# Kernel optimization log

Measured on AMD Instinct MI355X. Metric: run time of the kernel, lower is better.

Reference implementation:

```python
import jax, jax.numpy as jnp
import numpy as np

N = 16384          # num nodes
E = 262144         # num edges (before self loops)
IN_DIM = 128
HID = 128
OUT = 2
TRIM = 0.1
MAX_DEG = 48       # padded max in-degree (incl. self loop); safe bound for Poisson(16)+1
BN_EPS = 1e-5


def _lin_params(key, fan_in, fan_out):
    kw, kb = jax.random.split(key)
    s = 1.0 / np.sqrt(fan_in)
    W = jax.random.uniform(kw, (fan_in, fan_out), jnp.float32, -s, s)
    b = jax.random.uniform(kb, (fan_out,), jnp.float32, -s, s)
    return W, b


def setup_inputs() -> dict:
    key = jax.random.key(0)
    ks = jax.random.split(key, 8)
    x = jax.random.normal(ks[0], (N, IN_DIM), jnp.float32)
    edge_index = jax.random.randint(ks[1], (2, E), 0, N, jnp.int32)
    Wl0, bl0 = _lin_params(ks[2], IN_DIM, HID)
    Wr0, br0 = _lin_params(ks[3], IN_DIM, HID)
    Wl1, bl1 = _lin_params(ks[4], HID, HID)
    Wr1, br1 = _lin_params(ks[5], HID, HID)
    Wl2, bl2 = _lin_params(ks[6], HID, OUT)
    Wr2, br2 = _lin_params(ks[7], HID, OUT)
    g0 = jnp.ones((HID,), jnp.float32); be0 = jnp.zeros((HID,), jnp.float32)
    g1 = jnp.ones((HID,), jnp.float32); be1 = jnp.zeros((HID,), jnp.float32)
    return dict(x=x, edge_index=edge_index,
                Wl0=Wl0, bl0=bl0, Wr0=Wr0, br0=br0, g0=g0, be0=be0,
                Wl1=Wl1, bl1=bl1, Wr1=Wr1, br1=br1, g1=g1, be1=be1,
                Wl2=Wl2, bl2=bl2, Wr2=Wr2, br2=br2)


def _forward(edge_index, x, Wl0, bl0, Wr0, br0, g0, be0,
             Wl1, bl1, Wr1, br1, g1, be1, Wl2, bl2, Wr2, br2):
    loops = jnp.arange(N, dtype=edge_index.dtype)
    row = jnp.concatenate([edge_index[0], loops])   # source nodes
    col = jnp.concatenate([edge_index[1], loops])   # destination nodes
    counts = jax.ops.segment_sum(jnp.ones_like(col), col, num_segments=N)  # in-degree, int
    deg = jnp.maximum(counts, 1).astype(x.dtype)
    norm = 1.0 / deg[col]                            # 1/deg(dst), per edge

    # Edge ordering grouped by destination node; rank = slot within the node's group.
    perm = jnp.argsort(col, stable=True)
    col_s = col[perm]
    starts = jnp.cumsum(counts) - counts
    rank = jnp.arange(col.shape[0], dtype=counts.dtype) - starts[col_s]
    node_id = jnp.where(rank < MAX_DEG, col_s, N)    # overflow slots -> OOB, dropped by scatter

    t = jnp.maximum(1, jnp.floor(counts.astype(jnp.float32) * TRIM).astype(counts.dtype))
    tcnt = counts - 2 * t
    pos = jnp.arange(MAX_DEG)[None, :]
    sel = (pos >= t[:, None]) & (pos < (counts - t)[:, None])   # [N, MAX_DEG]
    use_trim = (counts >= 5) & (tcnt > 0)
    inv_tcnt = 1.0 / jnp.maximum(tcnt, 1).astype(x.dtype)

    def trimmed_scatter(msg):
        # plain mean fallback
        mean = jax.ops.segment_sum(msg, col, num_segments=N) / deg[:, None]
        d = msg.shape[1]
        # padded per-node buffer; +inf pads sort to the end (never selected by `sel`)
        dense = jnp.full((N, MAX_DEG, d), jnp.inf, msg.dtype)
        dense = dense.at[node_id, rank].set(msg[perm], mode='drop')
        sdense = jnp.sort(dense, axis=1)             # per-feature sort within each node
        tmean = jnp.sum(jnp.where(sel[:, :, None], sdense, 0.0), axis=1) * inv_tcnt[:, None]
        return jnp.where(use_trim[:, None], tmean, mean)

    def conv(h, Wl, bl, Wr, br):
        msg = (h @ Wl + bl)[row] * norm[:, None]
        return trimmed_scatter(msg) + h @ Wr + br

    bn_scale = jnp.float32(1.0 / np.sqrt(1.0 + BN_EPS))  # eval-mode BN: running mean 0, var 1
    h = conv(x, Wl0, bl0, Wr0, br0)
    h = jax.nn.relu(h * bn_scale * g0 + be0)
    h = conv(h, Wl1, bl1, Wr1, br1)
    h = jax.nn.relu(h * bn_scale * g1 + be1)
    return conv(h, Wl2, bl2, Wr2, br2)


def reference(x, edge_index, Wl0, bl0, Wr0, br0, g0, be0,
              Wl1, bl1, Wr1, br1, g1, be1, Wl2, bl2, Wr2, br2):
    return _forward(edge_index, x, Wl0, bl0, Wr0, br0, g0, be0,
                    Wl1, bl1, Wr1, br1, g1, be1, Wl2, bl2, Wr2, br2)
```

## Files before the change

### kernel.cpp

```cpp
#include <hip/hip_runtime.h>
#include <hip/hip_bf16.h>
#include <math.h>

#define GN    16384
#define HID   128
#define MAXD  48
#define BN_SCALE 0.9999950000374998f

typedef __attribute__((ext_vector_type(8))) short short8;
typedef __attribute__((ext_vector_type(4))) float f32x4;

__device__ inline short f2bf(float x) {
    unsigned u = __float_as_uint(x);
    unsigned r = (u + 0x7fffu + ((u >> 16) & 1u)) >> 16;
    return (short)r;
}
__device__ inline float bf2f(short s) {
    return __uint_as_float(((unsigned)(unsigned short)s) << 16);
}

__global__ __launch_bounds__(256) void k_prep(
    int* __restrict__ adj, int* __restrict__ fill,
    const float* __restrict__ Wl0, const float* __restrict__ Wr0,
    const float* __restrict__ Wl1, const float* __restrict__ Wr1,
    short* __restrict__ W5)
{
    int t = blockIdx.x * 256 + threadIdx.x;
    fill[t] = 1;
    adj[t * MAXD] = t;

    int layer = t >> 13;
    int g     = t & 8191;
    int split = (g >> 12) & 1;
    int ks    = (g >> 10) & 3;
    int nt    = (g >> 6) & 15;
    int l     = g & 63;
    int q = l >> 4, r = l & 15;
    int n = nt * 16 + r;
    const float* Wl = layer ? Wl1 : Wl0;
    const float* Wr = layer ? Wr1 : Wr0;
    const float* W  = (n < 128) ? Wl : Wr;
    int ncol = (n < 128) ? n : (n - 128);

    short8 out;
    #pragma unroll
    for (int j = 0; j < 8; ++j) {
        int k = ks * 32 + (j >> 2) * 16 + q * 4 + (j & 3);
        float wv = W[k * 128 + ncol];
        short hi = f2bf(wv);
        short val = split ? f2bf(wv - bf2f(hi)) : hi;
        out[j] = val;
    }
    *reinterpret_cast<short8*>(W5 + ((size_t)layer * 8192 + g) * 8) = out;
}

__global__ __launch_bounds__(256) void k_build(const int* __restrict__ src,
                                               const int* __restrict__ dst,
                                               int* __restrict__ adj,
                                               int* __restrict__ fill, int E) {
    int e = blockIdx.x * 256 + threadIdx.x;
    if (e < E) {
        int dv = dst[e];
        int slot = atomicAdd(&fill[dv], 1);
        if (slot < MAXD) adj[dv * MAXD + slot] = src[e];
    }
}

__global__ __launch_bounds__(256, 1) void k_gemm(
    const float* __restrict__ X, const short* __restrict__ W5,
    const float* __restrict__ bl, const float* __restrict__ br,
    float* __restrict__ C)
{
    const int tid = threadIdx.x;
    const int w = tid >> 6, l = tid & 63;
    const int q = l >> 4, r = l & 15;
    const int rowA = blockIdx.x * 64 + w * 16 + r;

    short ahi[8][4], alo[8][4];
    const float4* xp = reinterpret_cast<const float4*>(X + (size_t)rowA * 128);
    #pragma unroll
    for (int h = 0; h < 8; ++h) {
        float4 v = xp[h * 4 + q];
        float xv[4] = {v.x, v.y, v.z, v.w};
        #pragma unroll
        for (int j = 0; j < 4; ++j) {
            short hi = f2bf(xv[j]);
            ahi[h][j] = hi;
            alo[h][j] = f2bf(xv[j] - bf2f(hi));
        }
    }

    f32x4 acc[16];
    #pragma unroll
    for (int nt = 0; nt < 16; ++nt) {
        int col = nt * 16 + r;
        float b = (nt < 8) ? bl[col] : br[col - 128];
        acc[nt] = (f32x4){b, b, b, b};
    }

    #pragma unroll
    for (int ks = 0; ks < 4; ++ks) {
        short8 Ahi, Alo;
        #pragma unroll
        for (int j = 0; j < 4; ++j) {
            Ahi[j] = ahi[2 * ks][j];     Ahi[j + 4] = ahi[2 * ks + 1][j];
            Alo[j] = alo[2 * ks][j];     Alo[j + 4] = alo[2 * ks + 1][j];
        }
        #pragma unroll
        for (int nt = 0; nt < 16; ++nt) {
            short8 Bhi = *reinterpret_cast<const short8*>(
                W5 + ((size_t)(ks * 16 + nt) * 64 + l) * 8);
            short8 Blo = *reinterpret_cast<const short8*>(
                W5 + ((size_t)((4 + ks) * 16 + nt) * 64 + l) * 8);
            acc[nt] = __builtin_amdgcn_mfma_f32_16x16x32_bf16(Ahi, Bhi, acc[nt], 0, 0, 0);
            acc[nt] = __builtin_amdgcn_mfma_f32_16x16x32_bf16(Ahi, Blo, acc[nt], 0, 0, 0);
            acc[nt] = __builtin_amdgcn_mfma_f32_16x16x32_bf16(Alo, Bhi, acc[nt], 0, 0, 0);
        }
    }

    const int rb = blockIdx.x * 64 + w * 16 + 4 * q;
    #pragma unroll
    for (int nt = 0; nt < 16; ++nt) {
        int col = nt * 16 + r;
        #pragma unroll
        for (int j = 0; j < 4; ++j)
            C[(size_t)(rb + j) * 256 + col] = acc[nt][j];
    }
}

struct F2 { float x, y; };
__device__ inline F2 f2min(F2 a, F2 b) { return {fminf(a.x, b.x), fminf(a.y, b.y)}; }
__device__ inline F2 f2max(F2 a, F2 b) { return {fmaxf(a.x, b.x), fmaxf(a.y, b.y)}; }

__global__ __launch_bounds__(256) void k_agg(
    const float* __restrict__ C,
    const int* __restrict__ adj, const int* __restrict__ fill,
    const float* __restrict__ g, const float* __restrict__ be,
    float* __restrict__ hb)
{
    __shared__ int sadj[4][MAXD];
    const int tid = threadIdx.x, w = tid >> 6, l = tid & 63;
    const int v = blockIdx.x * 4 + w;
    const int cnt = fill[v];
    const int d = min(cnt, MAXD);
    if (l < d) sadj[w][l] = adj[v * MAXD + l] * 256;
    __syncthreads();

    const int f2 = l * 2;
    F2 tot = {0.f, 0.f};
    F2 s0 = { INFINITY,  INFINITY}, s1 = s0, s2 = s0, s3 = s0;
    F2 l0 = {-INFINITY, -INFINITY}, l1 = l0, l2 = l0, l3 = l0;

    if (cnt < 20) {
        for (int i = 0; i < d; ++i) {
            const float2 xv = *reinterpret_cast<const float2*>(C + sadj[w][i] + f2);
            F2 x = {xv.x, xv.y};
            tot.x += x.x; tot.y += x.y;
            s0 = f2min(s0, x);
            l0 = f2max(l0, x);
        }
    } else {
        for (int i = 0; i < d; ++i) {
            const float2 xv = *reinterpret_cast<const float2*>(C + sadj[w][i] + f2);
            F2 x = {xv.x, xv.y};
            tot.x += x.x; tot.y += x.y;
            F2 a = x;
            F2 t0 = f2min(s0, a); a = f2max(s0, a); s0 = t0;
            F2 t1 = f2min(s1, a); a = f2max(s1, a); s1 = t1;
            F2 t2 = f2min(s2, a); a = f2max(s2, a); s2 = t2;
            s3 = f2min(s3, a);
            F2 b = x;
            F2 u0 = f2max(l0, b); b = f2min(l0, b); l0 = u0;
            F2 u1 = f2max(l1, b); b = f2min(l1, b); l1 = u1;
            F2 u2 = f2max(l2, b); b = f2min(l2, b); l2 = u2;
            l3 = f2max(l3, b);
        }
    }

    int t = (int)floorf((float)cnt * 0.1f);
    if (t < 1) t = 1;
    int tcnt = cnt - 2 * t;
    bool use_trim = (cnt >= 5) && (tcnt > 0);
    float dd = (float)cnt;
    F2 res;
    if (use_trim) {
        int tt = min(t, 4);
        F2 bot = s0, top = l0;
        if (tt > 1) { bot.x += s1.x; bot.y += s1.y; top.x += l1.x; top.y += l1.y; }
        if (tt > 2) { bot.x += s2.x; bot.y += s2.y; top.x += l2.x; top.y += l2.y; }
        if (tt > 3) { bot.x += s3.x; bot.y += s3.y; top.x += l3.x; top.y += l3.y; }
        float inv = 1.0f / (dd * (float)tcnt);
        res.x = (tot.x - bot.x - top.x) * inv;
        res.y = (tot.y - bot.y - top.y) * inv;
    } else {
        float inv = 1.0f / (dd * dd);
        res.x = tot.x * inv;
        res.y = tot.y * inv;
    }

    const float2 hrv = *reinterpret_cast<const float2*>(C + (size_t)v * 256 + 128 + f2);
    float v0 = res.x + hrv.x;
    float v1 = res.y + hrv.y;
    v0 = fmaxf(v0 * (BN_SCALE * g[f2])     + be[f2],     0.f);
    v1 = fmaxf(v1 * (BN_SCALE * g[f2 + 1]) + be[f2 + 1], 0.f);
    float2 o = {v0, v1};
    *reinterpret_cast<float2*>(hb + (size_t)v * 128 + f2) = o;
}

__global__ __launch_bounds__(256) void k_gemm_out(
    const float* __restrict__ H,
    const float* __restrict__ Wl, const float* __restrict__ bl,
    const float* __restrict__ Wr, const float* __restrict__ br,
    float* __restrict__ Cl, float* __restrict__ Cr)
{
    int v = blockIdx.x * 256 + threadIdx.x;
    const float4* h = reinterpret_cast<const float4*>(H + (size_t)v * 128);
    float a0 = 0.f, a1 = 0.f, r0 = 0.f, r1 = 0.f;
    #pragma unroll
    for (int k4 = 0; k4 < 32; ++k4) {
        float4 hv = h[k4];
        float xs[4] = {hv.x, hv.y, hv.z, hv.w};
        #pragma unroll
        for (int c = 0; c < 4; ++c) {
            int k = 4 * k4 + c;
            a0 = fmaf(xs[c], Wl[k * 2 + 0], a0);
            a1 = fmaf(xs[c], Wl[k * 2 + 1], a1);
            r0 = fmaf(xs[c], Wr[k * 2 + 0], r0);
            r1 = fmaf(xs[c], Wr[k * 2 + 1], r1);
        }
    }
    Cl[v * 2 + 0] = a0 + bl[0];
    Cl[v * 2 + 1] = a1 + bl[1];
    Cr[v * 2 + 0] = r0 + br[0];
    Cr[v * 2 + 1] = r1 + br[1];
}

__global__ __launch_bounds__(256) void k_agg_out(
    const float* __restrict__ hl2, const float* __restrict__ hr2,
    const int* __restrict__ adj, const int* __restrict__ fill,
    float* __restrict__ out)
{
    int idx = blockIdx.x * 256 + threadIdx.x;
    int v = idx >> 1, j = idx & 1;
    int cnt = fill[v];
    int d = min(cnt, MAXD);
    const int* ap = adj + v * MAXD;

    float total = 0.f;
    float s0 = INFINITY, s1 = INFINITY, s2 = INFINITY, s3 = INFINITY;
    float l0 = -INFINITY, l1 = -INFINITY, l2 = -INFINITY, l3 = -INFINITY;
    for (int i = 0; i < d; ++i) {
        float x = hl2[ap[i] * 2 + j];
        total += x;
        float a = x;
        float t0 = fminf(s0, a); a = fmaxf(s0, a); s0 = t0;
        float t1 = fminf(s1, a); a = fmaxf(s1, a); s1 = t1;
        float t2 = fminf(s2, a); a = fmaxf(s2, a); s2 = t2;
        s3 = fminf(s3, a);
        float b = x;
        float u0 = fmaxf(l0, b); b = fminf(l0, b); l0 = u0;
        float u1 = fmaxf(l1, b); b = fminf(l1, b); l1 = u1;
        float u2 = fmaxf(l2, b); b = fminf(l2, b); l2 = u2;
        l3 = fmaxf(l3, b);
    }

    int t = (int)floorf((float)cnt * 0.1f);
    if (t < 1) t = 1;
    int tcnt = cnt - 2 * t;
    bool use_trim = (cnt >= 5) && (tcnt > 0);
    float dd = (float)cnt;
    float res;
    if (use_trim) {
        int tt = min(t, 4);
        float bot = s0, top = l0;
        if (tt > 1) { bot += s1; top += l1; }
        if (tt > 2) { bot += s2; top += l2; }
        if (tt > 3) { bot += s3; top += l3; }
        res = (total - bot - top) / (dd * (float)tcnt);
    } else {
        res = total / (dd * dd);
    }
    out[idx] = res + hr2[idx];
}

extern "C" void kernel_launch(void* const* d_in, const int* in_sizes, int n_in,
                              void* d_out, int out_size, void* d_ws, size_t ws_size,
                              hipStream_t stream)
{
    const float* x   = (const float*)d_in[0];
    const int*   ei  = (const int*)d_in[1];
    const int    E   = in_sizes[1] / 2;
    const float* Wl0 = (const float*)d_in[2];
    const float* bl0 = (const float*)d_in[3];
    const float* Wr0 = (const float*)d_in[4];
    const float* br0 = (const float*)d_in[5];
    const float* g0  = (const float*)d_in[6];
    const float* be0 = (const float*)d_in[7];
    const float* Wl1 = (const float*)d_in[8];
    const float* bl1 = (const float*)d_in[9];
    const float* Wr1 = (const float*)d_in[10];
    const float* br1 = (const float*)d_in[11];
    const float* g1  = (const float*)d_in[12];
    const float* be1 = (const float*)d_in[13];
    const float* Wl2 = (const float*)d_in[14];
    const float* bl2 = (const float*)d_in[15];
    const float* Wr2 = (const float*)d_in[16];
    const float* br2 = (const float*)d_in[17];
    float* out = (float*)d_out;

    char* w = (char*)d_ws;
    int*   adj  = (int*)w;    w += (size_t)GN * MAXD * 4;
    int*   fill = (int*)w;    w += (size_t)GN * 4;
    float* C    = (float*)w;  w += (size_t)GN * 256 * 4;
    float* hb   = (float*)w;  w += (size_t)GN * 128 * 4;
    short* W5   = (short*)w;  w += (size_t)2 * 8192 * 16;
    float* hl2  = (float*)w;  w += (size_t)GN * 2 * 4;
    float* hr2  = (float*)w;  w += (size_t)GN * 2 * 4;

    k_prep <<<GN / 256, 256, 0, stream>>>(adj, fill, Wl0, Wr0, Wl1, Wr1, W5);
    k_build<<<(E + 255) / 256, 256, 0, stream>>>(ei, ei + E, adj, fill, E);

    k_gemm<<<GN / 64, 256, 0, stream>>>(x, W5, bl0, br0, C);
    k_agg <<<GN / 4, 256, 0, stream>>>(C, adj, fill, g0, be0, hb);
    k_gemm<<<GN / 64, 256, 0, stream>>>(hb, W5 + (size_t)8192 * 8, bl1, br1, C);
    k_agg <<<GN / 4, 256, 0, stream>>>(C, adj, fill, g1, be1, hb);
    k_gemm_out<<<GN / 256, 256, 0, stream>>>(hb, Wl2, bl2, Wr2, br2, hl2, hr2);
    k_agg_out<<<GN * 2 / 256, 256, 0, stream>>>(hl2, hr2, adj, fill, out);
}
```

Before: 210.0 us.

## Store gathered messages in fp16, split GEMM tiles, fuse graph build and prep

The message half of the GEMM output (h@Wl+b) is now stored in fp16 in its own buffer and the root term in fp32, so the per-edge gather in aggregation reads half the bytes. The GEMM is split so each block covers 32 rows and each wave covers half the columns, with launch bounds set to 2 blocks per SM. Adjacency build, self-loop insertion and weight packing are merged into one kernel after a memset, which removes a launch. The final small GEMM uses two threads per node. Self loops are now inserted by atomics, so their slot order within a node is no longer fixed. Storing messages in fp16 lowers their precision and may affect accuracy.

```diff
diff --git a/kernel.cpp b/kernel.cpp
--- a/kernel.cpp
+++ b/kernel.cpp
@@ -1,130 +1,133 @@
 #include <hip/hip_runtime.h>
 #include <hip/hip_bf16.h>
+#include <hip/hip_fp16.h>
 #include <math.h>
 
 #define GN    16384
-#define HID   128
 #define MAXD  48
 #define BN_SCALE 0.9999950000374998f
 
 typedef __attribute__((ext_vector_type(8))) short short8;
 typedef __attribute__((ext_vector_type(4))) float f32x4;
+typedef _Float16 __attribute__((ext_vector_type(2))) h2v;
 
 __device__ inline short f2bf(float x) {
     unsigned u = __float_as_uint(x);
-    unsigned r = (u + 0x7fffu + ((u >> 16) & 1u)) >> 16;
-    return (short)r;
+    return (short)((u + 0x7fffu + ((u >> 16) & 1u)) >> 16);
 }
 __device__ inline float bf2f(short s) {
     return __uint_as_float(((unsigned)(unsigned short)s) << 16);
 }
 
-__global__ __launch_bounds__(256) void k_prep(
+__global__ __launch_bounds__(256) void k_build(
+    const int* __restrict__ src, const int* __restrict__ dst, int E,
     int* __restrict__ adj, int* __restrict__ fill,
     const float* __restrict__ Wl0, const float* __restrict__ Wr0,
     const float* __restrict__ Wl1, const float* __restrict__ Wr1,
     short* __restrict__ W5)
 {
-    int t = blockIdx.x * 256 + threadIdx.x;
-    fill[t] = 1;
-    adj[t * MAXD] = t;
-
-    int layer = t >> 13;
-    int g     = t & 8191;
+    int idx = blockIdx.x * 256 + threadIdx.x;
+    if (idx < E) {
+        int dv = dst[idx];
+        int slot = atomicAdd(&fill[dv], 1);
+        if (slot < MAXD) adj[dv * MAXD + slot] = src[idx];
+        return;
+    }
+    idx -= E;
+    if (idx < GN) {
+        int slot = atomicAdd(&fill[idx], 1);
+        if (slot < MAXD) adj[idx * MAXD + slot] = idx;
+        return;
+    }
+    idx -= GN;
+    if (idx >= 2 * 8192) return;
+    int layer = idx >> 13;
+    int g     = idx & 8191;
     int split = (g >> 12) & 1;
     int ks    = (g >> 10) & 3;
     int nt    = (g >> 6) & 15;
     int l     = g & 63;
     int q = l >> 4, r = l & 15;
     int n = nt * 16 + r;
-    const float* Wl = layer ? Wl1 : Wl0;
-    const float* Wr = layer ? Wr1 : Wr0;
-    const float* W  = (n < 128) ? Wl : Wr;
-    int ncol = (n < 128) ? n : (n - 128);
-
+    const float* W = (n < 128) ? (layer ? Wl1 : Wl0) : (layer ? Wr1 : Wr0);
+    int ncol = n & 127;
     short8 out;
     #pragma unroll
     for (int j = 0; j < 8; ++j) {
         int k = ks * 32 + (j >> 2) * 16 + q * 4 + (j & 3);
         float wv = W[k * 128 + ncol];
         short hi = f2bf(wv);
-        short val = split ? f2bf(wv - bf2f(hi)) : hi;
-        out[j] = val;
+        out[j] = split ? f2bf(wv - bf2f(hi)) : hi;
     }
     *reinterpret_cast<short8*>(W5 + ((size_t)layer * 8192 + g) * 8) = out;
 }
 
-__global__ __launch_bounds__(256) void k_build(const int* __restrict__ src,
-                                               const int* __restrict__ dst,
-                                               int* __restrict__ adj,
-                                               int* __restrict__ fill, int E) {
-    int e = blockIdx.x * 256 + threadIdx.x;
-    if (e < E) {
-        int dv = dst[e];
-        int slot = atomicAdd(&fill[dv], 1);
-        if (slot < MAXD) adj[dv * MAXD + slot] = src[e];
-    }
-}
-
-__global__ __launch_bounds__(256, 1) void k_gemm(
+__global__ __launch_bounds__(256, 2) void k_gemm(
     const float* __restrict__ X, const short* __restrict__ W5,
     const float* __restrict__ bl, const float* __restrict__ br,
-    float* __restrict__ C)
+    _Float16* __restrict__ HL, float* __restrict__ HR)
 {
     const int tid = threadIdx.x;
     const int w = tid >> 6, l = tid & 63;
     const int q = l >> 4, r = l & 15;
-    const int rowA = blockIdx.x * 64 + w * 16 + r;
-
-    short ahi[8][4], alo[8][4];
+    const int half = w & 1, nhalf = w >> 1;
+    const int rowA = blockIdx.x * 32 + half * 16 + r;
+
+    short8 Ahi[4], Alo[4];
     const float4* xp = reinterpret_cast<const float4*>(X + (size_t)rowA * 128);
     #pragma unroll
     for (int h = 0; h < 8; ++h) {
         float4 v = xp[h * 4 + q];
         float xv[4] = {v.x, v.y, v.z, v.w};
+        int ks = h >> 1, hk = h & 1;
         #pragma unroll
         for (int j = 0; j < 4; ++j) {
             short hi = f2bf(xv[j]);
-            ahi[h][j] = hi;
-            alo[h][j] = f2bf(xv[j] - bf2f(hi));
-        }
-    }
-
-    f32x4 acc[16];
-    #pragma unroll
-    for (int nt = 0; nt < 16; ++nt) {
-        int col = nt * 16 + r;
-        float b = (nt < 8) ? bl[col] : br[col - 128];
+            Ahi[ks][hk * 4 + j] = hi;
+            Alo[ks][hk * 4 + j] = f2bf(xv[j] - bf2f(hi));
+        }
+    }
+
+    const float* bias = nhalf ? br : bl;
+    f32x4 acc[8];
+    #pragma unroll
+    for (int nt = 0; nt < 8; ++nt) {
+        float b = bias[nt * 16 + r];
         acc[nt] = (f32x4){b, b, b, b};
     }
 
     #pragma unroll
     for (int ks = 0; ks < 4; ++ks) {
-        short8 Ahi, Alo;
-        #pragma unroll
-        for (int j = 0; j < 4; ++j) {
-            Ahi[j] = ahi[2 * ks][j];     Ahi[j + 4] = ahi[2 * ks + 1][j];
-            Alo[j] = alo[2 * ks][j];     Alo[j + 4] = alo[2 * ks + 1][j];
-        }
-        #pragma unroll
-        for (int nt = 0; nt < 16; ++nt) {
+        #pragma unroll
+        for (int nt = 0; nt < 8; ++nt) {
+            int ntg = nhalf * 8 + nt;
             short8 Bhi = *reinterpret_cast<const short8*>(
-                W5 + ((size_t)(ks * 16 + nt) * 64 + l) * 8);
+                W5 + ((size_t)((ks) * 16 + ntg) * 64 + l) * 8);
             short8 Blo = *reinterpret_cast<const short8*>(
-                W5 + ((size_t)((4 + ks) * 16 + nt) * 64 + l) * 8);
-            acc[nt] = __builtin_amdgcn_mfma_f32_16x16x32_bf16(Ahi, Bhi, acc[nt], 0, 0, 0);
-            acc[nt] = __builtin_amdgcn_mfma_f32_16x16x32_bf16(Ahi, Blo, acc[nt], 0, 0, 0);
-            acc[nt] = __builtin_amdgcn_mfma_f32_16x16x32_bf16(Alo, Bhi, acc[nt], 0, 0, 0);
-        }
-    }
-
-    const int rb = blockIdx.x * 64 + w * 16 + 4 * q;
-    #pragma unroll
-    for (int nt = 0; nt < 16; ++nt) {
-        int col = nt * 16 + r;
-        #pragma unroll
-        for (int j = 0; j < 4; ++j)
-            C[(size_t)(rb + j) * 256 + col] = acc[nt][j];
+                W5 + ((size_t)((4 + ks) * 16 + ntg) * 64 + l) * 8);
+            acc[nt] = __builtin_amdgcn_mfma_f32_16x16x32_bf16(Ahi[ks], Bhi, acc[nt], 0, 0, 0);
+            acc[nt] = __builtin_amdgcn_mfma_f32_16x16x32_bf16(Ahi[ks], Blo, acc[nt], 0, 0, 0);
+            acc[nt] = __builtin_amdgcn_mfma_f32_16x16x32_bf16(Alo[ks], Bhi, acc[nt], 0, 0, 0);
+        }
+    }
+
+    const int rb = blockIdx.x * 32 + half * 16 + 4 * q;
+    if (nhalf == 0) {
+        #pragma unroll
+        for (int nt = 0; nt < 8; ++nt) {
+            int c = nt * 16 + r;
+            #pragma unroll
+            for (int j = 0; j < 4; ++j)
+                HL[(size_t)(rb + j) * 128 + c] = (_Float16)acc[nt][j];
+        }
+    } else {
+        #pragma unroll
+        for (int nt = 0; nt < 8; ++nt) {
+            int c = nt * 16 + r;
+            #pragma unroll
+            for (int j = 0; j < 4; ++j)
+                HR[(size_t)(rb + j) * 128 + c] = acc[nt][j];
+        }
     }
 }
 
@@ -133,7 +136,7 @@
 __device__ inline F2 f2max(F2 a, F2 b) { return {fmaxf(a.x, b.x), fmaxf(a.y, b.y)}; }
 
 __global__ __launch_bounds__(256) void k_agg(
-    const float* __restrict__ C,
+    const _Float16* __restrict__ HL, const float* __restrict__ HR,
     const int* __restrict__ adj, const int* __restrict__ fill,
     const float* __restrict__ g, const float* __restrict__ be,
     float* __restrict__ hb)
@@ -143,26 +146,26 @@
     const int v = blockIdx.x * 4 + w;
     const int cnt = fill[v];
     const int d = min(cnt, MAXD);
-    if (l < d) sadj[w][l] = adj[v * MAXD + l] * 256;
+    if (l < d) sadj[w][l] = adj[v * MAXD + l] * 128;
     __syncthreads();
 
-    const int f2 = l * 2;
+    const int f2i = l * 2;
     F2 tot = {0.f, 0.f};
     F2 s0 = { INFINITY,  INFINITY}, s1 = s0, s2 = s0, s3 = s0;
     F2 l0 = {-INFINITY, -INFINITY}, l1 = l0, l2 = l0, l3 = l0;
 
     if (cnt < 20) {
         for (int i = 0; i < d; ++i) {
-            const float2 xv = *reinterpret_cast<const float2*>(C + sadj[w][i] + f2);
-            F2 x = {xv.x, xv.y};
+            h2v hv = *reinterpret_cast<const h2v*>(HL + sadj[w][i] + f2i);
+            F2 x = {(float)hv[0], (float)hv[1]};
             tot.x += x.x; tot.y += x.y;
             s0 = f2min(s0, x);
             l0 = f2max(l0, x);
         }
     } else {
         for (int i = 0; i < d; ++i) {
-            const float2 xv = *reinterpret_cast<const float2*>(C + sadj[w][i] + f2);
-            F2 x = {xv.x, xv.y};
+            h2v hv = *reinterpret_cast<const h2v*>(HL + sadj[w][i] + f2i);
+            F2 x = {(float)hv[0], (float)hv[1]};
             tot.x += x.x; tot.y += x.y;
             F2 a = x;
             F2 t0 = f2min(s0, a); a = f2max(s0, a); s0 = t0;
@@ -198,24 +201,23 @@
         res.y = tot.y * inv;
     }
 
-    const float2 hrv = *reinterpret_cast<const float2*>(C + (size_t)v * 256 + 128 + f2);
-    float v0 = res.x + hrv.x;
-    float v1 = res.y + hrv.y;
-    v0 = fmaxf(v0 * (BN_SCALE * g[f2])     + be[f2],     0.f);
-    v1 = fmaxf(v1 * (BN_SCALE * g[f2 + 1]) + be[f2 + 1], 0.f);
+    const float2 hrv = *reinterpret_cast<const float2*>(HR + (size_t)v * 128 + f2i);
+    float v0 = fmaxf((res.x + hrv.x) * (BN_SCALE * g[f2i])     + be[f2i],     0.f);
+    float v1 = fmaxf((res.y + hrv.y) * (BN_SCALE * g[f2i + 1]) + be[f2i + 1], 0.f);
     float2 o = {v0, v1};
-    *reinterpret_cast<float2*>(hb + (size_t)v * 128 + f2) = o;
+    *reinterpret_cast<float2*>(hb + (size_t)v * 128 + f2i) = o;
 }
 
 __global__ __launch_bounds__(256) void k_gemm_out(
     const float* __restrict__ H,
     const float* __restrict__ Wl, const float* __restrict__ bl,
     const float* __restrict__ Wr, const float* __restrict__ br,
-    float* __restrict__ Cl, float* __restrict__ Cr)
-{
-    int v = blockIdx.x * 256 + threadIdx.x;
+    float* __restrict__ hl2, float* __restrict__ hr2)
+{
+    int idx = blockIdx.x * 256 + threadIdx.x;
+    int v = idx >> 1, j = idx & 1;
     const float4* h = reinterpret_cast<const float4*>(H + (size_t)v * 128);
-    float a0 = 0.f, a1 = 0.f, r0 = 0.f, r1 = 0.f;
+    float a = 0.f, rr = 0.f;
     #pragma unroll
     for (int k4 = 0; k4 < 32; ++k4) {
         float4 hv = h[k4];
@@ -223,16 +225,12 @@
         #pragma unroll
         for (int c = 0; c < 4; ++c) {
             int k = 4 * k4 + c;
-            a0 = fmaf(xs[c], Wl[k * 2 + 0], a0);
-            a1 = fmaf(xs[c], Wl[k * 2 + 1], a1);
-            r0 = fmaf(xs[c], Wr[k * 2 + 0], r0);
-            r1 = fmaf(xs[c], Wr[k * 2 + 1], r1);
-        }
-    }
-    Cl[v * 2 + 0] = a0 + bl[0];
-    Cl[v * 2 + 1] = a1 + bl[1];
-    Cr[v * 2 + 0] = r0 + br[0];
-    Cr[v * 2 + 1] = r1 + br[1];
+            a  = fmaf(xs[c], Wl[k * 2 + j], a);
+            rr = fmaf(xs[c], Wr[k * 2 + j], rr);
+        }
+    }
+    hl2[idx] = a + bl[j];
+    hr2[idx] = rr + br[j];
 }
 
 __global__ __launch_bounds__(256) void k_agg_out(
@@ -309,21 +307,26 @@
     float* out = (float*)d_out;
 
     char* w = (char*)d_ws;
-    int*   adj  = (int*)w;    w += (size_t)GN * MAXD * 4;
-    int*   fill = (int*)w;    w += (size_t)GN * 4;
-    float* C    = (float*)w;  w += (size_t)GN * 256 * 4;
-    float* hb   = (float*)w;  w += (size_t)GN * 128 * 4;
-    short* W5   = (short*)w;  w += (size_t)2 * 8192 * 16;
-    float* hl2  = (float*)w;  w += (size_t)GN * 2 * 4;
-    float* hr2  = (float*)w;  w += (size_t)GN * 2 * 4;
-
-    k_prep <<<GN / 256, 256, 0, stream>>>(adj, fill, Wl0, Wr0, Wl1, Wr1, W5);
-    k_build<<<(E + 255) / 256, 256, 0, stream>>>(ei, ei + E, adj, fill, E);
-
-    k_gemm<<<GN / 64, 256, 0, stream>>>(x, W5, bl0, br0, C);
-    k_agg <<<GN / 4, 256, 0, stream>>>(C, adj, fill, g0, be0, hb);
-    k_gemm<<<GN / 64, 256, 0, stream>>>(hb, W5 + (size_t)8192 * 8, bl1, br1, C);
-    k_agg <<<GN / 4, 256, 0, stream>>>(C, adj, fill, g1, be1, hb);
-    k_gemm_out<<<GN / 256, 256, 0, stream>>>(hb, Wl2, bl2, Wr2, br2, hl2, hr2);
-    k_agg_out<<<GN * 2 / 256, 256, 0, stream>>>(hl2, hr2, adj, fill, out);
-}
+    int*      adj  = (int*)w;       w += (size_t)GN * MAXD * 4;
+    int*      fill = (int*)w;       w += (size_t)GN * 4;
+    _Float16* HL   = (_Float16*)w;  w += (size_t)GN * 128 * 2;
+    float*    HR   = (float*)w;     w += (size_t)GN * 128 * 4;
+    float*    hb   = (float*)w;     w += (size_t)GN * 128 * 4;
+    short*    W5   = (short*)w;     w += (size_t)2 * 8192 * 16;
+    float*    hl2  = (float*)w;     w += (size_t)GN * 2 * 4;
+    float*    hr2  = (float*)w;     w += (size_t)GN * 2 * 4;
+
+    hipMemsetAsync(fill, 0, (size_t)GN * 4, stream);
+    {
+        int total = E + GN + 2 * 8192;
+        k_build<<<(total + 255) / 256, 256, 0, stream>>>(
+            ei, ei + E, E, adj, fill, Wl0, Wr0, Wl1, Wr1, W5);
+    }
+
+    k_gemm<<<GN / 32, 256, 0, stream>>>(x, W5, bl0, br0, HL, HR);
+    k_agg <<<GN / 4, 256, 0, stream>>>(HL, HR, adj, fill, g0, be0, hb);
+    k_gemm<<<GN / 32, 256, 0, stream>>>(hb, W5 + (size_t)8192 * 8, bl1, br1, HL, HR);
+    k_agg <<<GN / 4, 256, 0, stream>>>(HL, HR, adj, fill, g1, be1, hb);
+    k_gemm_out<<<GN * 2 / 256, 256, 0, stream>>>(hb, Wl2, bl2, Wr2, br2, hl2, hr2);
+    k_agg_out <<<GN * 2 / 256, 256, 0, stream>>>(hl2, hr2, adj, fill, out);
+}
```

Result: faster. 200.2 us (-4.7%).
